# Optimization experiments

Measured on AMD Instinct MI355X. Metric: run time of the kernel, lower is better.

## Reference

```python
import jax, jax.numpy as jnp
import numpy as np

B, S, H, V, E = 64, 20, 128, 50257, 300


def gru(p, x, h):
    # tf.contrib.rnn.GRUCell: r,u = sigmoid([x,h]@Wg + bg); c = tanh([x, r*h]@Wc + bc); h' = u*h + (1-u)*c
    gk, gb, ck, cb = p
    xh = jnp.concatenate([x, h], axis=-1)
    r, u = jnp.split(jax.nn.sigmoid(xh @ gk + gb), 2, axis=-1)
    c = jnp.tanh(jnp.concatenate([x, r * h], axis=-1) @ ck + cb)
    return u * h + (1.0 - u) * c


def setup_inputs() -> dict:
    key = jax.random.key(0)
    ks = jax.random.split(key, 32)
    s = 0.08
    rn = lambda k, shp: (jax.random.normal(k, shp, jnp.float32) * s)
    inp = {}
    inp['x'] = jax.random.randint(ks[0], (B, S), 0, V, dtype=jnp.int32)
    inp['x_length'] = jax.random.randint(ks[1], (B,), 1, S + 1, dtype=jnp.int32)
    inp['y'] = jax.random.randint(ks[2], (B, S), 0, V, dtype=jnp.int32)
    inp['y_length'] = jax.random.randint(ks[3], (B,), 1, S + 1, dtype=jnp.int32)
    inp['embedding'] = jax.random.normal(ks[4], (V, E), jnp.float32) * 0.1
    # encoder GRU: layer0 in=E, layer1 in=H
    inp['e0_gk'] = rn(ks[5], (E + H, 2 * H)); inp['e0_gb'] = rn(ks[6], (2 * H,))
    inp['e0_ck'] = rn(ks[7], (E + H, H));     inp['e0_cb'] = rn(ks[8], (H,))
    inp['e1_gk'] = rn(ks[9], (2 * H, 2 * H)); inp['e1_gb'] = rn(ks[10], (2 * H,))
    inp['e1_ck'] = rn(ks[11], (2 * H, H));    inp['e1_cb'] = rn(ks[12], (H,))
    # decoder GRU: layer0 in = E + attention_size(H) = E+H, layer1 in=H
    inp['d0_gk'] = rn(ks[13], (E + 2 * H, 2 * H)); inp['d0_gb'] = rn(ks[14], (2 * H,))
    inp['d0_ck'] = rn(ks[15], (E + 2 * H, H));     inp['d0_cb'] = rn(ks[16], (H,))
    inp['d1_gk'] = rn(ks[17], (2 * H, 2 * H));     inp['d1_gb'] = rn(ks[18], (2 * H,))
    inp['d1_ck'] = rn(ks[19], (2 * H, H));         inp['d1_cb'] = rn(ks[20], (H,))
    # Bahdanau attention (num_units=H) + attention output layer + vocab projection
    inp['W_mem'] = rn(ks[21], (H, H))
    inp['W_q'] = rn(ks[22], (H, H))
    inp['v_att'] = rn(ks[23], (H,))
    inp['W_attn'] = rn(ks[24], (2 * H, H))
    inp['W_proj'] = rn(ks[25], (H, V))
    inp['b_proj'] = jnp.zeros((V,), jnp.float32)
    return inp


def _forward(x, x_length, y, y_length, embedding,
             e0_gk, e0_gb, e0_ck, e0_cb, e1_gk, e1_gb, e1_ck, e1_cb,
             d0_gk, d0_gb, d0_ck, d0_cb, d1_gk, d1_gb, d1_ck, d1_cb,
             W_mem, W_q, v_att, W_attn, W_proj, b_proj):
    e0 = (e0_gk, e0_gb, e0_ck, e0_cb)
    e1 = (e1_gk, e1_gb, e1_ck, e1_cb)
    d0 = (d0_gk, d0_gb, d0_ck, d0_cb)
    d1 = (d1_gk, d1_gb, d1_ck, d1_cb)
    t_idx = jnp.arange(S)
    x_valid = t_idx[None, :] < x_length[:, None]   # [B,S]
    y_valid = t_idx[None, :] < y_length[:, None]   # [B,S]

    # ---- encoder: 2-layer GRU dynamic_rnn with sequence_length semantics ----
    ex = embedding[x]                               # [B,S,E]
    zeros = jnp.zeros((x.shape[0], H), embedding.dtype)

    def enc_step(carry, inp_t):
        h0, h1 = carry
        xt, vt = inp_t                              # xt [B,E], vt [B,1]
        n0 = gru(e0, xt, h0)
        n1 = gru(e1, n0, h1)
        n0 = jnp.where(vt, n0, h0)                  # copy-through past seq end
        n1 = jnp.where(vt, n1, h1)
        return (n0, n1), jnp.where(vt, n1, 0.0)     # outputs zeroed past seq end

    (h0f, h1f), mem = jax.lax.scan(
        enc_step, (zeros, zeros),
        (ex.transpose(1, 0, 2), x_valid.T[:, :, None]))
    memory = mem.transpose(1, 0, 2)                 # [B,S,H] encoder outputs

    # ---- Bahdanau attention precompute ----
    keys = jnp.einsum('bsh,hu->bsu', memory, W_mem)  # memory_layer(memory)
    neg_inf = jnp.finfo(memory.dtype).min

    # ---- attention decoder (TrainingHelper) ----
    ey = embedding[y]                               # [B,S,E]
    attn0 = jnp.zeros((x.shape[0], H), embedding.dtype)

    def dec_step(carry, inp_t):
        h0, h1, attn = carry
        yt, vt = inp_t                              # yt [B,E], vt [B,1]
        ci = jnp.concatenate([yt, attn], axis=-1)   # cell input = [emb, prev attention]
        n0 = gru(d0, ci, h0)
        n1 = gru(d1, n0, h1)
        q = n1 @ W_q                                # query_layer(cell_output)
        sc = jnp.einsum('bsu,u->bs', jnp.tanh(keys + q[:, None, :]), v_att)
        sc = jnp.where(x_valid, sc, neg_inf)        # memory_sequence_length mask
        al = jax.nn.softmax(sc, axis=-1)            # [B,S]
        ctx = jnp.einsum('bs,bsh->bh', al, memory)  # context
        na = jnp.concatenate([n1, ctx], axis=-1) @ W_attn  # attention_layer (no bias)
        logits = na @ W_proj + b_proj               # projection_layer
        logits = jnp.where(vt, logits, 0.0)         # dynamic_decode zeroes finished emits
        return (n0, n1, na), logits

    _, logits = jax.lax.scan(
        dec_step, (h0f, h1f, attn0),
        (ey.transpose(1, 0, 2), y_valid.T[:, :, None]))
    return logits.transpose(1, 0, 2)                # [B,S,V] rnn_output


def reference(x, x_length, y, y_length, embedding,
              e0_gk, e0_gb, e0_ck, e0_cb, e1_gk, e1_gb, e1_ck, e1_cb,
              d0_gk, d0_gb, d0_ck, d0_cb, d1_gk, d1_gb, d1_ck, d1_cb,
              W_mem, W_q, v_att, W_attn, W_proj, b_proj):
    return _forward(x, x_length, y, y_length, embedding,
                    e0_gk, e0_gb, e0_ck, e0_cb, e1_gk, e1_gb, e1_ck, e1_cb,
                    d0_gk, d0_gb, d0_ck, d0_cb, d1_gk, d1_gb, d1_ck, d1_cb,
                    W_mem, W_q, v_att, W_attn, W_proj, b_proj)
```

## Files before the change

### kernel.cpp

```cpp
#include <hip/hip_runtime.h>
#include <hip/hip_bf16.h>

#define Bb 64
#define Ss 20
#define Hh 128
#define Vv 50257
#define Ee 300
#define Vpad 50304

typedef short bf16x8 __attribute__((ext_vector_type(8)));
typedef float f32x4 __attribute__((ext_vector_type(4)));

__device__ __forceinline__ unsigned short f2bf(float f){
  unsigned u = __float_as_uint(f);
  u += 0x7fff + ((u >> 16) & 1);
  return (unsigned short)(u >> 16);
}
__device__ __forceinline__ float sigm(float x){ return 1.f / (1.f + __expf(-x)); }
__device__ __forceinline__ float tanh_fast(float x){
  float e = __expf(2.f * x);
  return 1.f - 2.f / (e + 1.f);
}

template<int K4>
__device__ __forceinline__ float dotT(const float* __restrict__ w, const float* v){
  float a0 = 0.f, a1 = 0.f, a2 = 0.f, a3 = 0.f;
  const float4* w4 = (const float4*)w;
  const float4* v4 = (const float4*)v;
#pragma unroll
  for (int i = 0; i < K4; i++){
    float4 wv = w4[i]; float4 xv = v4[i];
    a0 = fmaf(wv.x, xv.x, a0); a1 = fmaf(wv.y, xv.y, a1);
    a2 = fmaf(wv.z, xv.z, a2); a3 = fmaf(wv.w, xv.w, a3);
  }
  return (a0 + a1) + (a2 + a3);
}


struct TMat { const float* src; float* dst; int r0, R, C; };
struct TList { TMat m[15]; };

__global__ __launch_bounds__(256) void wtrans_kernel(TList L){
  TMat t = L.m[blockIdx.y];
  int idx = blockIdx.x * 256 + threadIdx.x;
  int total = t.R * t.C;
  if (idx >= total) return;
  int o = idx / t.R;
  int i = idx - o * t.R;
  t.dst[idx] = t.src[(size_t)(t.r0 + i) * t.C + o];
}

__global__ __launch_bounds__(256) void wpt_kernel(const float* __restrict__ Wp,
                                                  unsigned short* __restrict__ Wpt){
  __shared__ unsigned short tile[64][136];
  int n0 = blockIdx.x * 64;
  int tid = threadIdx.x;
  for (int idx = tid; idx < 8192; idx += 256){
    int k = idx >> 6, nn = idx & 63;
    int n = n0 + nn;
    float f = (n < Vv) ? Wp[(size_t)k * Vv + n] : 0.f;
    tile[nn][k] = f2bf(f);
  }
  __syncthreads();
  for (int idx = tid; idx < 1024; idx += 256){
    int nn = idx >> 4, c = idx & 15;
    uint4 v = *reinterpret_cast<const uint4*>(&tile[nn][c * 8]);
    *reinterpret_cast<uint4*>(Wpt + (((size_t)(n0 + nn)) << 7) + c * 8) = v;
  }
}


__global__ __launch_bounds__(256) void pre_kernel(
    const int* __restrict__ x, const int* __restrict__ y, const float* __restrict__ emb,
    const float* __restrict__ egx, const float* __restrict__ ecx,
    const float* __restrict__ egb, const float* __restrict__ ecb,
    const float* __restrict__ dgx, const float* __restrict__ dcx,
    const float* __restrict__ dgb, const float* __restrict__ dcb,
    float* __restrict__ epg, float* __restrict__ epc,
    float* __restrict__ dpg, float* __restrict__ dpc)
{
  __shared__ __align__(16) float er[Ee];
  int tid = threadIdx.x, ti = blockIdx.x, which = blockIdx.y;
  int tok = which ? y[ti] : x[ti];
  if (tid < 75)
    ((float4*)er)[tid] = ((const float4*)(emb + (size_t)tok * Ee))[tid];
  __syncthreads();
  const float* gx = which ? dgx : egx;
  const float* cx = which ? dcx : ecx;
  float accg = (which ? dgb : egb)[tid] + dotT<75>(gx + (size_t)tid * Ee, er);
  (which ? dpg : epg)[ti * 256 + tid] = accg;
  if (tid < 128){
    float accc = (which ? dcb : ecb)[tid] + dotT<75>(cx + (size_t)tid * Ee, er);
    (which ? dpc : epc)[ti * 128 + tid] = accc;
  }
}


__global__ __launch_bounds__(256, 1) void recur2(
    const int* __restrict__ xlen,
    const float* __restrict__ epg, const float* __restrict__ epc,
    const float* __restrict__ dpg, const float* __restrict__ dpc,
    const float* __restrict__ e0_gh_t, const float* __restrict__ e0_ch_t,
    const float* __restrict__ e1_g_t, const float* __restrict__ e1_c_t,
    const float* __restrict__ e1_gb,  const float* __restrict__ e1_cb,
    const float* __restrict__ d0_gah_t, const float* __restrict__ d0_cah_t,
    const float* __restrict__ d1_g_t, const float* __restrict__ d1_c_t,
    const float* __restrict__ d1_gb,  const float* __restrict__ d1_cb,
    const float* __restrict__ W_mem_t, const float* __restrict__ W_q_t,
    const float* __restrict__ W_attn_t, const float* __restrict__ v_att,
    unsigned short* __restrict__ na_bf)
{
  __shared__ __align__(16) float mem_s[Ss][Hh];
  __shared__ __align__(16) float keys_s[Ss][132];
  __shared__ __align__(16) float h0[Hh], h1[Hh], attn[Hh], n0[Hh], n1[Hh], rh[Hh], q[Hh], ctx[Hh];
  __shared__ __align__(16) float gates[2*Hh];
  __shared__ __align__(16) float vatt_s[Hh];
  __shared__ float part[Ss][8], als[Ss];

  const int tid = threadIdx.x, b = blockIdx.x;
  if (tid < Hh){ h0[tid] = 0.f; h1[tid] = 0.f; attn[tid] = 0.f; vatt_s[tid] = v_att[tid]; }
  __syncthreads();
  const int xl = xlen[b];

  for (int t = 0; t < Ss; t++){
    const int tix = b * Ss + t;
    {
      float g = epg[(tix << 8) + tid] + dotT<32>(e0_gh_t + tid * 128, h0);
      float sg = sigm(g);
      if (tid < Hh) rh[tid] = sg * h0[tid];
      else          gates[tid] = sg;
    }
    __syncthreads();
    {
      int o = tid >> 1, half = tid & 1;
      float a = dotT<16>(e0_ch_t + o * 128 + half * 64, rh + half * 64);
      a += __shfl_xor(a, 1);
      if (!half){
        float c = tanh_fast(epc[(tix << 7) + o] + a);
        float u = gates[128 + o];
        n0[o] = u * h0[o] + (1.f - u) * c;
      }
    }
    __syncthreads();
    {
      float g1 = e1_gb[tid] + dotT<32>(e1_g_t + tid * 256, n0)
                            + dotT<32>(e1_g_t + tid * 256 + 128, h1);
      float sg = sigm(g1);
      if (tid < Hh) rh[tid] = sg * h1[tid];
      else          gates[tid] = sg;
    }
    __syncthreads();
    {
      int o = tid >> 1, half = tid & 1;
      const float* base = e1_c_t + o * 256 + half * 128;
      float a = half ? dotT<32>(base, rh) : dotT<32>(base, n0);
      a += __shfl_xor(a, 1);
      if (!half){
        float c = tanh_fast(e1_cb[o] + a);
        float u = gates[128 + o];
        float nh = u * h1[o] + (1.f - u) * c;
        bool v = (t < xl);
        mem_s[t][o] = v ? nh : 0.f;
        h1[o] = v ? nh : h1[o];
        h0[o] = v ? n0[o] : h0[o];
      }
    }
    __syncthreads();
  }

  for (int idx = tid; idx < Ss * Hh; idx += 256){
    int s = idx >> 7, j = idx & 127;
    keys_s[s][j] = dotT<32>(W_mem_t + j * 128, mem_s[s]);
  }
  __syncthreads();

  for (int t = 0; t < Ss; t++){
    const int tix = b * Ss + t;
    {
      float g = dpg[(tix << 8) + tid] + dotT<32>(d0_gah_t + tid * 256, attn)
                                      + dotT<32>(d0_gah_t + tid * 256 + 128, h0);
      float sg = sigm(g);
      if (tid < Hh) rh[tid] = sg * h0[tid];
      else          gates[tid] = sg;
    }
    __syncthreads();
    {
      int o = tid >> 1, half = tid & 1;
      const float* base = d0_cah_t + o * 256 + half * 128;
      float a = half ? dotT<32>(base, rh) : dotT<32>(base, attn);
      a += __shfl_xor(a, 1);
      if (!half){
        float c = tanh_fast(dpc[(tix << 7) + o] + a);
        float u = gates[128 + o];
        float nv = u * h0[o] + (1.f - u) * c;
        n0[o] = nv; h0[o] = nv;
      }
    }
    __syncthreads();
    {
      float g1 = d1_gb[tid] + dotT<32>(d1_g_t + tid * 256, n0)
                            + dotT<32>(d1_g_t + tid * 256 + 128, h1);
      float sg = sigm(g1);
      if (tid < Hh) rh[tid] = sg * h1[tid];
      else          gates[tid] = sg;
    }
    __syncthreads();
    {
      int o = tid >> 1, half = tid & 1;
      const float* base = d1_c_t + o * 256 + half * 128;
      float a = half ? dotT<32>(base, rh) : dotT<32>(base, n0);
      a += __shfl_xor(a, 1);
      if (!half){
        float c = tanh_fast(d1_cb[o] + a);
        float u = gates[128 + o];
        float nh = u * h1[o] + (1.f - u) * c;
        n1[o] = nh; h1[o] = nh;
      }
    }
    __syncthreads();
    {
      int o = tid >> 1, half = tid & 1;
      float a = dotT<16>(W_q_t + o * 128 + half * 64, n1 + half * 64);
      a += __shfl_xor(a, 1);
      if (!half) q[o] = a;
    }
    __syncthreads();
    if (tid < Ss * 8){
      int s = tid >> 3, p = tid & 7;
      float a = 0.f;
#pragma unroll
      for (int c2 = 0; c2 < 16; c2++){
        int u2 = p * 16 + c2;
        a += tanh_fast(keys_s[s][u2] + q[u2]) * vatt_s[u2];
      }
      part[s][p] = a;
    }
    __syncthreads();
    if (tid < 64){
      int s = tid;
      bool valid = (s < Ss) && (s < xl);
      float sc = -3.4e38f;
      if (valid){ sc = 0.f;
#pragma unroll
        for (int p = 0; p < 8; p++) sc += part[s][p];
      }
      float mx = sc;
#pragma unroll
      for (int off = 32; off >= 1; off >>= 1) mx = fmaxf(mx, __shfl_xor(mx, off));
      float e = valid ? __expf(sc - mx) : 0.f;
      float sm = e;
#pragma unroll
      for (int off = 32; off >= 1; off >>= 1) sm += __shfl_xor(sm, off);
      if (s < Ss) als[s] = e / sm;
    }
    __syncthreads();
    if (tid < Hh){
      float a = 0.f;
#pragma unroll
      for (int s = 0; s < Ss; s++) a += als[s] * mem_s[s][tid];
      ctx[tid] = a;
    }
    __syncthreads();
    {
      int o = tid >> 1, half = tid & 1;
      const float* base = W_attn_t + o * 256 + half * 128;
      float a = half ? dotT<32>(base, ctx) : dotT<32>(base, n1);
      a += __shfl_xor(a, 1);
      if (!half){
        attn[o] = a;
        na_bf[(tix << 7) + o] = f2bf(a);
      }
    }
    __syncthreads();
  }
}


__global__ __launch_bounds__(256) void proj2(
    const unsigned short* __restrict__ na_bf, const unsigned short* __restrict__ Wpt,
    const float* __restrict__ b_proj, const int* __restrict__ ylen,
    float* __restrict__ out)
{
  __shared__ int yl_s[Bb];
  const int tid = threadIdx.x;
  if (tid < Bb) yl_s[tid] = ylen[tid];
  const int n0 = blockIdx.x * 128, m0 = blockIdx.y * 64;
  const int lane = tid & 63, w = tid >> 6, lm = lane & 15, qq = lane >> 4;

  f32x4 acc[4][2];
#pragma unroll
  for (int mt = 0; mt < 4; mt++){ acc[mt][0] = (f32x4){0,0,0,0}; acc[mt][1] = (f32x4){0,0,0,0}; }

#pragma unroll
  for (int ks = 0; ks < 4; ks++){
    int ko = ks * 32 + qq * 8;
    bf16x8 b0 = *(const bf16x8*)(Wpt + (((size_t)(n0 + w*32 + lm)) << 7) + ko);
    bf16x8 b1 = *(const bf16x8*)(Wpt + (((size_t)(n0 + w*32 + 16 + lm)) << 7) + ko);
#pragma unroll
    for (int mt = 0; mt < 4; mt++){
      bf16x8 a = *(const bf16x8*)(na_bf + (((size_t)(m0 + mt*16 + lm)) << 7) + ko);
      acc[mt][0] = __builtin_amdgcn_mfma_f32_16x16x32_bf16(a, b0, acc[mt][0], 0, 0, 0);
      acc[mt][1] = __builtin_amdgcn_mfma_f32_16x16x32_bf16(a, b1, acc[mt][1], 0, 0, 0);
    }
  }
  __syncthreads();

#pragma unroll
  for (int mt = 0; mt < 4; mt++){
    int row = m0 + mt*16 + qq*4;
#pragma unroll
    for (int n2 = 0; n2 < 2; n2++){
      int col = n0 + w*32 + n2*16 + lm;
      if (col < Vv){
        float bp = b_proj[col];
#pragma unroll
        for (int r = 0; r < 4; r++){
          int rr = row + r;
          int bb = rr / Ss;
          int tt = rr - bb * Ss;
          float val = (tt < yl_s[bb]) ? (acc[mt][n2][r] + bp) : 0.f;
          out[(size_t)rr * Vv + col] = val;
        }
      }
    }
  }
}

extern "C" void kernel_launch(void* const* d_in, const int* in_sizes, int n_in,
                              void* d_out, int out_size, void* d_ws, size_t ws_size,
                              hipStream_t stream) {
  const int*   x        = (const int*)d_in[0];
  const int*   x_length = (const int*)d_in[1];
  const int*   y        = (const int*)d_in[2];
  const int*   y_length = (const int*)d_in[3];
  const float* emb      = (const float*)d_in[4];
  const float* e0_gk = (const float*)d_in[5];  const float* e0_gb = (const float*)d_in[6];
  const float* e0_ck = (const float*)d_in[7];  const float* e0_cb = (const float*)d_in[8];
  const float* e1_gk = (const float*)d_in[9];  const float* e1_gb = (const float*)d_in[10];
  const float* e1_ck = (const float*)d_in[11]; const float* e1_cb = (const float*)d_in[12];
  const float* d0_gk = (const float*)d_in[13]; const float* d0_gb = (const float*)d_in[14];
  const float* d0_ck = (const float*)d_in[15]; const float* d0_cb = (const float*)d_in[16];
  const float* d1_gk = (const float*)d_in[17]; const float* d1_gb = (const float*)d_in[18];
  const float* d1_ck = (const float*)d_in[19]; const float* d1_cb = (const float*)d_in[20];
  const float* W_mem = (const float*)d_in[21]; const float* W_q   = (const float*)d_in[22];
  const float* v_att = (const float*)d_in[23]; const float* W_attn= (const float*)d_in[24];
  const float* W_proj= (const float*)d_in[25]; const float* b_proj= (const float*)d_in[26];
  float* out = (float*)d_out;

  size_t off = 0;
  auto alloc = [&](size_t bytes) -> void* {
    void* p = (char*)d_ws + off;
    off += (bytes + 255) & ~(size_t)255;
    return p;
  };
  unsigned short* Wpt   = (unsigned short*)alloc((size_t)Vpad * 128 * 2);
  unsigned short* na_bf = (unsigned short*)alloc((size_t)Bb * Ss * Hh * 2);
  float* epg = (float*)alloc((size_t)Bb*Ss*256*4);
  float* epc = (float*)alloc((size_t)Bb*Ss*128*4);
  float* dpg = (float*)alloc((size_t)Bb*Ss*256*4);
  float* dpc = (float*)alloc((size_t)Bb*Ss*128*4);
  float* e0_gx_t  = (float*)alloc(256*300*4);
  float* e0_gh_t  = (float*)alloc(256*128*4);
  float* e0_cx_t  = (float*)alloc(128*300*4);
  float* e0_ch_t  = (float*)alloc(128*128*4);
  float* e1_g_t   = (float*)alloc(256*256*4);
  float* e1_c_t   = (float*)alloc(128*256*4);
  float* d0_gx_t  = (float*)alloc(256*300*4);
  float* d0_gah_t = (float*)alloc(256*256*4);
  float* d0_cx_t  = (float*)alloc(128*300*4);
  float* d0_cah_t = (float*)alloc(128*256*4);
  float* d1_g_t   = (float*)alloc(256*256*4);
  float* d1_c_t   = (float*)alloc(128*256*4);
  float* W_mem_t  = (float*)alloc(128*128*4);
  float* W_q_t    = (float*)alloc(128*128*4);
  float* W_attn_t = (float*)alloc(128*256*4);

  TList L;
  L.m[0]  = { e0_gk, e0_gx_t,    0, 300, 256 };
  L.m[1]  = { e0_gk, e0_gh_t,  300, 128, 256 };
  L.m[2]  = { e0_ck, e0_cx_t,    0, 300, 128 };
  L.m[3]  = { e0_ck, e0_ch_t,  300, 128, 128 };
  L.m[4]  = { e1_gk, e1_g_t,     0, 256, 256 };
  L.m[5]  = { e1_ck, e1_c_t,     0, 256, 128 };
  L.m[6]  = { d0_gk, d0_gx_t,    0, 300, 256 };
  L.m[7]  = { d0_gk, d0_gah_t, 300, 256, 256 };
  L.m[8]  = { d0_ck, d0_cx_t,    0, 300, 128 };
  L.m[9]  = { d0_ck, d0_cah_t, 300, 256, 128 };
  L.m[10] = { d1_gk, d1_g_t,     0, 256, 256 };
  L.m[11] = { d1_ck, d1_c_t,     0, 256, 128 };
  L.m[12] = { W_mem, W_mem_t,    0, 128, 128 };
  L.m[13] = { W_q,   W_q_t,      0, 128, 128 };
  L.m[14] = { W_attn,W_attn_t,   0, 256, 128 };

  wtrans_kernel<<<dim3(300, 15), 256, 0, stream>>>(L);
  wpt_kernel<<<Vpad / 64, 256, 0, stream>>>(W_proj, Wpt);
  pre_kernel<<<dim3(Bb * Ss, 2), 256, 0, stream>>>(
      x, y, emb, e0_gx_t, e0_cx_t, e0_gb, e0_cb,
      d0_gx_t, d0_cx_t, d0_gb, d0_cb, epg, epc, dpg, dpc);
  recur2<<<Bb, 256, 0, stream>>>(
      x_length, epg, epc, dpg, dpc,
      e0_gh_t, e0_ch_t, e1_g_t, e1_c_t, e1_gb, e1_cb,
      d0_gah_t, d0_cah_t, d1_g_t, d1_c_t, d1_gb, d1_cb,
      W_mem_t, W_q_t, W_attn_t, v_att, na_bf);
  proj2<<<dim3(Vpad / 128, (Bb * Ss) / 64), 256, 0, stream>>>(
      na_bf, Wpt, b_proj, y_length, out);
}
```

Baseline: 1.331 ms.

## Double recurrence block to 512 threads and fuse softmax into context step

The sequential GRU/attention recurrence kernel now runs with 512 threads per block. Each matvec is split across two or four threads per output with shuffle reductions, which shortens the per-thread dot-product chain on the serial critical path. The separate softmax stage with its barrier is removed, and each context thread now recomputes max, exp and sum redundantly. This saves a sync per decoder step at the cost of duplicated work and more wavefronts per block.

```diff
diff --git a/kernel.cpp b/kernel.cpp
--- a/kernel.cpp
+++ b/kernel.cpp
@@ -96,7 +96,7 @@
 }
 
 
-__global__ __launch_bounds__(256, 1) void recur2(
+__global__ __launch_bounds__(512, 1) void recur2(
     const int* __restrict__ xlen,
     const float* __restrict__ epg, const float* __restrict__ epc,
     const float* __restrict__ dpg, const float* __restrict__ dpc,
@@ -115,60 +115,67 @@
   __shared__ __align__(16) float h0[Hh], h1[Hh], attn[Hh], n0[Hh], n1[Hh], rh[Hh], q[Hh], ctx[Hh];
   __shared__ __align__(16) float gates[2*Hh];
   __shared__ __align__(16) float vatt_s[Hh];
-  __shared__ float part[Ss][8], als[Ss];
+  __shared__ float part[Ss][8];
 
   const int tid = threadIdx.x, b = blockIdx.x;
   if (tid < Hh){ h0[tid] = 0.f; h1[tid] = 0.f; attn[tid] = 0.f; vatt_s[tid] = v_att[tid]; }
   __syncthreads();
   const int xl = xlen[b];
 
+  const int o2 = tid >> 1, hf = tid & 1;
+  const int o4 = tid >> 2, qu = tid & 3;
+
   for (int t = 0; t < Ss; t++){
     const int tix = b * Ss + t;
     {
-      float g = epg[(tix << 8) + tid] + dotT<32>(e0_gh_t + tid * 128, h0);
-      float sg = sigm(g);
-      if (tid < Hh) rh[tid] = sg * h0[tid];
-      else          gates[tid] = sg;
-    }
-    __syncthreads();
-    {
-      int o = tid >> 1, half = tid & 1;
-      float a = dotT<16>(e0_ch_t + o * 128 + half * 64, rh + half * 64);
+      float a = dotT<16>(e0_gh_t + o2 * 128 + hf * 64, h0 + hf * 64);
       a += __shfl_xor(a, 1);
-      if (!half){
-        float c = tanh_fast(epc[(tix << 7) + o] + a);
-        float u = gates[128 + o];
-        n0[o] = u * h0[o] + (1.f - u) * c;
-      }
-    }
-    __syncthreads();
-    {
-      float g1 = e1_gb[tid] + dotT<32>(e1_g_t + tid * 256, n0)
-                            + dotT<32>(e1_g_t + tid * 256 + 128, h1);
-      float sg = sigm(g1);
-      if (tid < Hh) rh[tid] = sg * h1[tid];
-      else          gates[tid] = sg;
-    }
-    __syncthreads();
-    {
-      int o = tid >> 1, half = tid & 1;
-      const float* base = e1_c_t + o * 256 + half * 128;
-      float a = half ? dotT<32>(base, rh) : dotT<32>(base, n0);
+      if (!hf){
+        float sg = sigm(epg[(tix << 8) + o2] + a);
+        if (o2 < Hh) rh[o2] = sg * h0[o2];
+        else         gates[o2] = sg;
+      }
+    }
+    __syncthreads();
+    {
+      float a = dotT<8>(e0_ch_t + o4 * 128 + qu * 32, rh + qu * 32);
+      a += __shfl_xor(a, 1); a += __shfl_xor(a, 2);
+      if (!qu){
+        float c = tanh_fast(epc[(tix << 7) + o4] + a);
+        float u = gates[128 + o4];
+        n0[o4] = u * h0[o4] + (1.f - u) * c;
+      }
+    }
+    __syncthreads();
+    {
+      const float* base = e1_g_t + o2 * 256 + hf * 128;
+      float a = hf ? dotT<32>(base, h1) : dotT<32>(base, n0);
       a += __shfl_xor(a, 1);
-      if (!half){
-        float c = tanh_fast(e1_cb[o] + a);
-        float u = gates[128 + o];
-        float nh = u * h1[o] + (1.f - u) * c;
-        bool v = (t < xl);
-        mem_s[t][o] = v ? nh : 0.f;
-        h1[o] = v ? nh : h1[o];
-        h0[o] = v ? n0[o] : h0[o];
-      }
-    }
-    __syncthreads();
-  }
-
-  for (int idx = tid; idx < Ss * Hh; idx += 256){
+      if (!hf){
+        float sg = sigm(e1_gb[o2] + a);
+        if (o2 < Hh) rh[o2] = sg * h1[o2];
+        else         gates[o2] = sg;
+      }
+    }
+    __syncthreads();
+    {
+      const float* v = (qu < 2) ? n0 : rh;
+      float a = dotT<16>(e1_c_t + o4 * 256 + qu * 64, v + (qu & 1) * 64);
+      a += __shfl_xor(a, 1); a += __shfl_xor(a, 2);
+      if (!qu){
+        float c = tanh_fast(e1_cb[o4] + a);
+        float u = gates[128 + o4];
+        float nh = u * h1[o4] + (1.f - u) * c;
+        bool vv = (t < xl);
+        mem_s[t][o4] = vv ? nh : 0.f;
+        h1[o4] = vv ? nh : h1[o4];
+        h0[o4] = vv ? n0[o4] : h0[o4];
+      }
+    }
+    __syncthreads();
+  }
+
+  for (int idx = tid; idx < Ss * Hh; idx += 512){
     int s = idx >> 7, j = idx & 127;
     keys_s[s][j] = dotT<32>(W_mem_t + j * 128, mem_s[s]);
   }
@@ -177,52 +184,55 @@
   for (int t = 0; t < Ss; t++){
     const int tix = b * Ss + t;
     {
-      float g = dpg[(tix << 8) + tid] + dotT<32>(d0_gah_t + tid * 256, attn)
-                                      + dotT<32>(d0_gah_t + tid * 256 + 128, h0);
-      float sg = sigm(g);
-      if (tid < Hh) rh[tid] = sg * h0[tid];
-      else          gates[tid] = sg;
-    }
-    __syncthreads();
-    {
-      int o = tid >> 1, half = tid & 1;
-      const float* base = d0_cah_t + o * 256 + half * 128;
-      float a = half ? dotT<32>(base, rh) : dotT<32>(base, attn);
+      const float* base = d0_gah_t + o2 * 256 + hf * 128;
+      float a = hf ? dotT<32>(base, h0) : dotT<32>(base, attn);
       a += __shfl_xor(a, 1);
-      if (!half){
-        float c = tanh_fast(dpc[(tix << 7) + o] + a);
-        float u = gates[128 + o];
-        float nv = u * h0[o] + (1.f - u) * c;
-        n0[o] = nv; h0[o] = nv;
-      }
-    }
-    __syncthreads();
-    {
-      float g1 = d1_gb[tid] + dotT<32>(d1_g_t + tid * 256, n0)
-                            + dotT<32>(d1_g_t + tid * 256 + 128, h1);
-      float sg = sigm(g1);
-      if (tid < Hh) rh[tid] = sg * h1[tid];
-      else          gates[tid] = sg;
-    }
-    __syncthreads();
-    {
-      int o = tid >> 1, half = tid & 1;
-      const float* base = d1_c_t + o * 256 + half * 128;
-      float a = half ? dotT<32>(base, rh) : dotT<32>(base, n0);
+      if (!hf){
+        float sg = sigm(dpg[(tix << 8) + o2] + a);
+        if (o2 < Hh) rh[o2] = sg * h0[o2];
+        else         gates[o2] = sg;
+      }
+    }
+    __syncthreads();
+    {
+      const float* v = (qu < 2) ? attn : rh;
+      float a = dotT<16>(d0_cah_t + o4 * 256 + qu * 64, v + (qu & 1) * 64);
+      a += __shfl_xor(a, 1); a += __shfl_xor(a, 2);
+      if (!qu){
+        float c = tanh_fast(dpc[(tix << 7) + o4] + a);
+        float u = gates[128 + o4];
+        float nv = u * h0[o4] + (1.f - u) * c;
+        n0[o4] = nv; h0[o4] = nv;
+      }
+    }
+    __syncthreads();
+    {
+      const float* base = d1_g_t + o2 * 256 + hf * 128;
+      float a = hf ? dotT<32>(base, h1) : dotT<32>(base, n0);
       a += __shfl_xor(a, 1);
-      if (!half){
-        float c = tanh_fast(d1_cb[o] + a);
-        float u = gates[128 + o];
-        float nh = u * h1[o] + (1.f - u) * c;
-        n1[o] = nh; h1[o] = nh;
-      }
-    }
-    __syncthreads();
-    {
-      int o = tid >> 1, half = tid & 1;
-      float a = dotT<16>(W_q_t + o * 128 + half * 64, n1 + half * 64);
-      a += __shfl_xor(a, 1);
-      if (!half) q[o] = a;
+      if (!hf){
+        float sg = sigm(d1_gb[o2] + a);
+        if (o2 < Hh) rh[o2] = sg * h1[o2];
+        else         gates[o2] = sg;
+      }
+    }
+    __syncthreads();
+    {
+      const float* v = (qu < 2) ? n0 : rh;
+      float a = dotT<16>(d1_c_t + o4 * 256 + qu * 64, v + (qu & 1) * 64);
+      a += __shfl_xor(a, 1); a += __shfl_xor(a, 2);
+      if (!qu){
+        float c = tanh_fast(d1_cb[o4] + a);
+        float u = gates[128 + o4];
+        float nh = u * h1[o4] + (1.f - u) * c;
+        n1[o4] = nh; h1[o4] = nh;
+      }
+    }
+    __syncthreads();
+    {
+      float a = dotT<8>(W_q_t + o4 * 128 + qu * 32, n1 + qu * 32);
+      a += __shfl_xor(a, 1); a += __shfl_xor(a, 2);
+      if (!qu) q[o4] = a;
     }
     __syncthreads();
     if (tid < Ss * 8){
@@ -236,39 +246,36 @@
       part[s][p] = a;
     }
     __syncthreads();
-    if (tid < 64){
-      int s = tid;
-      bool valid = (s < Ss) && (s < xl);
-      float sc = -3.4e38f;
-      if (valid){ sc = 0.f;
-#pragma unroll
-        for (int p = 0; p < 8; p++) sc += part[s][p];
-      }
-      float mx = sc;
-#pragma unroll
-      for (int off = 32; off >= 1; off >>= 1) mx = fmaxf(mx, __shfl_xor(mx, off));
-      float e = valid ? __expf(sc - mx) : 0.f;
-      float sm = e;
-#pragma unroll
-      for (int off = 32; off >= 1; off >>= 1) sm += __shfl_xor(sm, off);
-      if (s < Ss) als[s] = e / sm;
-    }
-    __syncthreads();
     if (tid < Hh){
+      float e_[Ss];
+      float mx = -3.4e38f;
+#pragma unroll
+      for (int s = 0; s < Ss; s++){
+        float v = ((part[s][0] + part[s][1]) + (part[s][2] + part[s][3]))
+                + ((part[s][4] + part[s][5]) + (part[s][6] + part[s][7]));
+        v = (s < xl) ? v : -3.4e38f;
+        e_[s] = v; mx = fmaxf(mx, v);
+      }
+      float sm = 0.f;
+#pragma unroll
+      for (int s = 0; s < Ss; s++){
+        float e = (s < xl) ? __expf(e_[s] - mx) : 0.f;
+        e_[s] = e; sm += e;
+      }
+      float inv = 1.f / sm;
       float a = 0.f;
 #pragma unroll
-      for (int s = 0; s < Ss; s++) a += als[s] * mem_s[s][tid];
-      ctx[tid] = a;
-    }
-    __syncthreads();
-    {
-      int o = tid >> 1, half = tid & 1;
-      const float* base = W_attn_t + o * 256 + half * 128;
-      float a = half ? dotT<32>(base, ctx) : dotT<32>(base, n1);
-      a += __shfl_xor(a, 1);
-      if (!half){
-        attn[o] = a;
-        na_bf[(tix << 7) + o] = f2bf(a);
+      for (int s = 0; s < Ss; s++) a = fmaf(e_[s], mem_s[s][tid], a);
+      ctx[tid] = a * inv;
+    }
+    __syncthreads();
+    {
+      const float* v = (qu < 2) ? n1 : ctx;
+      float a = dotT<16>(W_attn_t + o4 * 256 + qu * 64, v + (qu & 1) * 64);
+      a += __shfl_xor(a, 1); a += __shfl_xor(a, 2);
+      if (!qu){
+        attn[o4] = a;
+        na_bf[(tix << 7) + o4] = f2bf(a);
       }
     }
     __syncthreads();
@@ -397,7 +404,7 @@
   pre_kernel<<<dim3(Bb * Ss, 2), 256, 0, stream>>>(
       x, y, emb, e0_gx_t, e0_cx_t, e0_gb, e0_cb,
       d0_gx_t, d0_cx_t, d0_gb, d0_cb, epg, epc, dpg, dpc);
-  recur2<<<Bb, 256, 0, stream>>>(
+  recur2<<<Bb, 512, 0, stream>>>(
       x_length, epg, epc, dpg, dpc,
       e0_gh_t, e0_ch_t, e1_g_t, e1_c_t, e1_gb, e1_cb,
       d0_gah_t, d0_cah_t, d1_g_t, d1_c_t, d1_gb, d1_cb,
```

After: 1.434 ms. 7.8% more time.

## Store recurrent weights in fp16 and fuse attention softmax into context step

Applied to the files above, without the earlier changes.

Recurrent and attention weight matrices are transposed into fp16 instead of fp32, and the sequential recurrence kernel reads them with 8-wide half loads converted to float. This halves the weight bytes streamed each timestep, which is meant to ease the latency- and bandwidth-bound serial loop. The attention softmax is also folded into the context computation, with each thread recomputing it redundantly, which removes one barrier per decoder step. The cost is reduced weight precision, which could shift numerics against the fp32 reference.

```diff
diff --git a/kernel.cpp b/kernel.cpp
--- a/kernel.cpp
+++ b/kernel.cpp
@@ -1,5 +1,6 @@
 #include <hip/hip_runtime.h>
 #include <hip/hip_bf16.h>
+#include <hip/hip_fp16.h>
 
 #define Bb 64
 #define Ss 20
@@ -10,6 +11,7 @@
 
 typedef short bf16x8 __attribute__((ext_vector_type(8)));
 typedef float f32x4 __attribute__((ext_vector_type(4)));
+typedef _Float16 h16x8 __attribute__((ext_vector_type(8)));
 
 __device__ __forceinline__ unsigned short f2bf(float f){
   unsigned u = __float_as_uint(f);
@@ -36,8 +38,25 @@
   return (a0 + a1) + (a2 + a3);
 }
 
-
-struct TMat { const float* src; float* dst; int r0, R, C; };
+template<int K8>
+__device__ __forceinline__ float dotH(const _Float16* __restrict__ w, const float* v){
+  float a0 = 0.f, a1 = 0.f, a2 = 0.f, a3 = 0.f;
+  const h16x8* w8 = (const h16x8*)w;
+  const float4* v4 = (const float4*)v;
+#pragma unroll
+  for (int i = 0; i < K8; i++){
+    h16x8 hv = w8[i];
+    float4 x0 = v4[2*i], x1 = v4[2*i+1];
+    a0 = fmaf((float)hv[0], x0.x, a0); a1 = fmaf((float)hv[1], x0.y, a1);
+    a2 = fmaf((float)hv[2], x0.z, a2); a3 = fmaf((float)hv[3], x0.w, a3);
+    a0 = fmaf((float)hv[4], x1.x, a0); a1 = fmaf((float)hv[5], x1.y, a1);
+    a2 = fmaf((float)hv[6], x1.z, a2); a3 = fmaf((float)hv[7], x1.w, a3);
+  }
+  return (a0 + a1) + (a2 + a3);
+}
+
+
+struct TMat { const float* src; void* dst; int r0, R, C, h; };
 struct TList { TMat m[15]; };
 
 __global__ __launch_bounds__(256) void wtrans_kernel(TList L){
@@ -47,7 +66,9 @@
   if (idx >= total) return;
   int o = idx / t.R;
   int i = idx - o * t.R;
-  t.dst[idx] = t.src[(size_t)(t.r0 + i) * t.C + o];
+  float val = t.src[(size_t)(t.r0 + i) * t.C + o];
+  if (t.h) ((_Float16*)t.dst)[idx] = (_Float16)val;
+  else     ((float*)t.dst)[idx]    = val;
 }
 
 __global__ __launch_bounds__(256) void wpt_kernel(const float* __restrict__ Wp,
@@ -100,14 +121,14 @@
     const int* __restrict__ xlen,
     const float* __restrict__ epg, const float* __restrict__ epc,
     const float* __restrict__ dpg, const float* __restrict__ dpc,
-    const float* __restrict__ e0_gh_t, const float* __restrict__ e0_ch_t,
-    const float* __restrict__ e1_g_t, const float* __restrict__ e1_c_t,
+    const _Float16* __restrict__ e0_gh_h, const _Float16* __restrict__ e0_ch_h,
+    const _Float16* __restrict__ e1_g_h, const _Float16* __restrict__ e1_c_h,
     const float* __restrict__ e1_gb,  const float* __restrict__ e1_cb,
-    const float* __restrict__ d0_gah_t, const float* __restrict__ d0_cah_t,
-    const float* __restrict__ d1_g_t, const float* __restrict__ d1_c_t,
+    const _Float16* __restrict__ d0_gah_h, const _Float16* __restrict__ d0_cah_h,
+    const _Float16* __restrict__ d1_g_h, const _Float16* __restrict__ d1_c_h,
     const float* __restrict__ d1_gb,  const float* __restrict__ d1_cb,
-    const float* __restrict__ W_mem_t, const float* __restrict__ W_q_t,
-    const float* __restrict__ W_attn_t, const float* __restrict__ v_att,
+    const _Float16* __restrict__ W_mem_h, const _Float16* __restrict__ W_q_h,
+    const _Float16* __restrict__ W_attn_h, const float* __restrict__ v_att,
     unsigned short* __restrict__ na_bf)
 {
   __shared__ __align__(16) float mem_s[Ss][Hh];
@@ -115,25 +136,25 @@
   __shared__ __align__(16) float h0[Hh], h1[Hh], attn[Hh], n0[Hh], n1[Hh], rh[Hh], q[Hh], ctx[Hh];
   __shared__ __align__(16) float gates[2*Hh];
   __shared__ __align__(16) float vatt_s[Hh];
-  __shared__ float part[Ss][8], als[Ss];
+  __shared__ float part[Ss][8];
 
   const int tid = threadIdx.x, b = blockIdx.x;
   if (tid < Hh){ h0[tid] = 0.f; h1[tid] = 0.f; attn[tid] = 0.f; vatt_s[tid] = v_att[tid]; }
   __syncthreads();
   const int xl = xlen[b];
+  const int o = tid >> 1, half = tid & 1;
 
   for (int t = 0; t < Ss; t++){
     const int tix = b * Ss + t;
     {
-      float g = epg[(tix << 8) + tid] + dotT<32>(e0_gh_t + tid * 128, h0);
+      float g = epg[(tix << 8) + tid] + dotH<16>(e0_gh_h + tid * 128, h0);
       float sg = sigm(g);
       if (tid < Hh) rh[tid] = sg * h0[tid];
       else          gates[tid] = sg;
     }
     __syncthreads();
     {
-      int o = tid >> 1, half = tid & 1;
-      float a = dotT<16>(e0_ch_t + o * 128 + half * 64, rh + half * 64);
+      float a = dotH<8>(e0_ch_h + o * 128 + half * 64, rh + half * 64);
       a += __shfl_xor(a, 1);
       if (!half){
         float c = tanh_fast(epc[(tix << 7) + o] + a);
@@ -143,17 +164,16 @@
     }
     __syncthreads();
     {
-      float g1 = e1_gb[tid] + dotT<32>(e1_g_t + tid * 256, n0)
-                            + dotT<32>(e1_g_t + tid * 256 + 128, h1);
+      float g1 = e1_gb[tid] + dotH<16>(e1_g_h + tid * 256, n0)
+                            + dotH<16>(e1_g_h + tid * 256 + 128, h1);
       float sg = sigm(g1);
       if (tid < Hh) rh[tid] = sg * h1[tid];
       else          gates[tid] = sg;
     }
     __syncthreads();
     {
-      int o = tid >> 1, half = tid & 1;
-      const float* base = e1_c_t + o * 256 + half * 128;
-      float a = half ? dotT<32>(base, rh) : dotT<32>(base, n0);
+      const _Float16* base = e1_c_h + o * 256 + half * 128;
+      float a = half ? dotH<16>(base, rh) : dotH<16>(base, n0);
       a += __shfl_xor(a, 1);
       if (!half){
         float c = tanh_fast(e1_cb[o] + a);
@@ -170,24 +190,23 @@
 
   for (int idx = tid; idx < Ss * Hh; idx += 256){
     int s = idx >> 7, j = idx & 127;
-    keys_s[s][j] = dotT<32>(W_mem_t + j * 128, mem_s[s]);
+    keys_s[s][j] = dotH<16>(W_mem_h + j * 128, mem_s[s]);
   }
   __syncthreads();
 
   for (int t = 0; t < Ss; t++){
     const int tix = b * Ss + t;
     {
-      float g = dpg[(tix << 8) + tid] + dotT<32>(d0_gah_t + tid * 256, attn)
-                                      + dotT<32>(d0_gah_t + tid * 256 + 128, h0);
+      float g = dpg[(tix << 8) + tid] + dotH<16>(d0_gah_h + tid * 256, attn)
+                                      + dotH<16>(d0_gah_h + tid * 256 + 128, h0);
       float sg = sigm(g);
       if (tid < Hh) rh[tid] = sg * h0[tid];
       else          gates[tid] = sg;
     }
     __syncthreads();
     {
-      int o = tid >> 1, half = tid & 1;
-      const float* base = d0_cah_t + o * 256 + half * 128;
-      float a = half ? dotT<32>(base, rh) : dotT<32>(base, attn);
+      const _Float16* base = d0_cah_h + o * 256 + half * 128;
+      float a = half ? dotH<16>(base, rh) : dotH<16>(base, attn);
       a += __shfl_xor(a, 1);
       if (!half){
         float c = tanh_fast(dpc[(tix << 7) + o] + a);
@@ -198,17 +217,16 @@
     }
     __syncthreads();
     {
-      float g1 = d1_gb[tid] + dotT<32>(d1_g_t + tid * 256, n0)
-                            + dotT<32>(d1_g_t + tid * 256 + 128, h1);
+      float g1 = d1_gb[tid] + dotH<16>(d1_g_h + tid * 256, n0)
+                            + dotH<16>(d1_g_h + tid * 256 + 128, h1);
       float sg = sigm(g1);
       if (tid < Hh) rh[tid] = sg * h1[tid];
       else          gates[tid] = sg;
     }
     __syncthreads();
     {
-      int o = tid >> 1, half = tid & 1;
-      const float* base = d1_c_t + o * 256 + half * 128;
-      float a = half ? dotT<32>(base, rh) : dotT<32>(base, n0);
+      const _Float16* base = d1_c_h + o * 256 + half * 128;
+      float a = half ? dotH<16>(base, rh) : dotH<16>(base, n0);
       a += __shfl_xor(a, 1);
       if (!half){
         float c = tanh_fast(d1_cb[o] + a);
@@ -219,8 +237,7 @@
     }
     __syncthreads();
     {
-      int o = tid >> 1, half = tid & 1;
-      float a = dotT<16>(W_q_t + o * 128 + half * 64, n1 + half * 64);
+      float a = dotH<8>(W_q_h + o * 128 + half * 64, n1 + half * 64);
       a += __shfl_xor(a, 1);
       if (!half) q[o] = a;
     }
@@ -236,35 +253,32 @@
       part[s][p] = a;
     }
     __syncthreads();
-    if (tid < 64){
-      int s = tid;
-      bool valid = (s < Ss) && (s < xl);
-      float sc = -3.4e38f;
-      if (valid){ sc = 0.f;
-#pragma unroll
-        for (int p = 0; p < 8; p++) sc += part[s][p];
-      }
-      float mx = sc;
-#pragma unroll
-      for (int off = 32; off >= 1; off >>= 1) mx = fmaxf(mx, __shfl_xor(mx, off));
-      float e = valid ? __expf(sc - mx) : 0.f;
-      float sm = e;
-#pragma unroll
-      for (int off = 32; off >= 1; off >>= 1) sm += __shfl_xor(sm, off);
-      if (s < Ss) als[s] = e / sm;
-    }
-    __syncthreads();
     if (tid < Hh){
+      float e_[Ss];
+      float mx = -3.4e38f;
+#pragma unroll
+      for (int s = 0; s < Ss; s++){
+        float v = ((part[s][0] + part[s][1]) + (part[s][2] + part[s][3]))
+                + ((part[s][4] + part[s][5]) + (part[s][6] + part[s][7]));
+        v = (s < xl) ? v : -3.4e38f;
+        e_[s] = v; mx = fmaxf(mx, v);
+      }
+      float sm = 0.f;
+#pragma unroll
+      for (int s = 0; s < Ss; s++){
+        float e = (s < xl) ? __expf(e_[s] - mx) : 0.f;
+        e_[s] = e; sm += e;
+      }
+      float inv = 1.f / sm;
       float a = 0.f;
 #pragma unroll
-      for (int s = 0; s < Ss; s++) a += als[s] * mem_s[s][tid];
-      ctx[tid] = a;
-    }
-    __syncthreads();
-    {
-      int o = tid >> 1, half = tid & 1;
-      const float* base = W_attn_t + o * 256 + half * 128;
-      float a = half ? dotT<32>(base, ctx) : dotT<32>(base, n1);
+      for (int s = 0; s < Ss; s++) a = fmaf(e_[s], mem_s[s][tid], a);
+      ctx[tid] = a * inv;
+    }
+    __syncthreads();
+    {
+      const _Float16* base = W_attn_h + o * 256 + half * 128;
+      float a = half ? dotH<16>(base, ctx) : dotH<16>(base, n1);
       a += __shfl_xor(a, 1);
       if (!half){
         attn[o] = a;
@@ -360,37 +374,37 @@
   float* dpg = (float*)alloc((size_t)Bb*Ss*256*4);
   float* dpc = (float*)alloc((size_t)Bb*Ss*128*4);
   float* e0_gx_t  = (float*)alloc(256*300*4);
-  float* e0_gh_t  = (float*)alloc(256*128*4);
   float* e0_cx_t  = (float*)alloc(128*300*4);
-  float* e0_ch_t  = (float*)alloc(128*128*4);
-  float* e1_g_t   = (float*)alloc(256*256*4);
-  float* e1_c_t   = (float*)alloc(128*256*4);
   float* d0_gx_t  = (float*)alloc(256*300*4);
-  float* d0_gah_t = (float*)alloc(256*256*4);
   float* d0_cx_t  = (float*)alloc(128*300*4);
-  float* d0_cah_t = (float*)alloc(128*256*4);
-  float* d1_g_t   = (float*)alloc(256*256*4);
-  float* d1_c_t   = (float*)alloc(128*256*4);
-  float* W_mem_t  = (float*)alloc(128*128*4);
-  float* W_q_t    = (float*)alloc(128*128*4);
-  float* W_attn_t = (float*)alloc(128*256*4);
+  _Float16* e0_gh_h  = (_Float16*)alloc(256*128*2);
+  _Float16* e0_ch_h  = (_Float16*)alloc(128*128*2);
+  _Float16* e1_g_h   = (_Float16*)alloc(256*256*2);
+  _Float16* e1_c_h   = (_Float16*)alloc(128*256*2);
+  _Float16* d0_gah_h = (_Float16*)alloc(256*256*2);
+  _Float16* d0_cah_h = (_Float16*)alloc(128*256*2);
+  _Float16* d1_g_h   = (_Float16*)alloc(256*256*2);
+  _Float16* d1_c_h   = (_Float16*)alloc(128*256*2);
+  _Float16* W_mem_h  = (_Float16*)alloc(128*128*2);
+  _Float16* W_q_h    = (_Float16*)alloc(128*128*2);
+  _Float16* W_attn_h = (_Float16*)alloc(128*256*2);
 
   TList L;
-  L.m[0]  = { e0_gk, e0_gx_t,    0, 300, 256 };
-  L.m[1]  = { e0_gk, e0_gh_t,  300, 128, 256 };
-  L.m[2]  = { e0_ck, e0_cx_t,    0, 300, 128 };
-  L.m[3]  = { e0_ck, e0_ch_t,  300, 128, 128 };
-  L.m[4]  = { e1_gk, e1_g_t,     0, 256, 256 };
-  L.m[5]  = { e1_ck, e1_c_t,     0, 256, 128 };
-  L.m[6]  = { d0_gk, d0_gx_t,    0, 300, 256 };
-  L.m[7]  = { d0_gk, d0_gah_t, 300, 256, 256 };
-  L.m[8]  = { d0_ck, d0_cx_t,    0, 300, 128 };
-  L.m[9]  = { d0_ck, d0_cah_t, 300, 256, 128 };
-  L.m[10] = { d1_gk, d1_g_t,     0, 256, 256 };
-  L.m[11] = { d1_ck, d1_c_t,     0, 256, 128 };
-  L.m[12] = { W_mem, W_mem_t,    0, 128, 128 };
-  L.m[13] = { W_q,   W_q_t,      0, 128, 128 };
-  L.m[14] = { W_attn,W_attn_t,   0, 256, 128 };
+  L.m[0]  = { e0_gk, e0_gx_t,    0, 300, 256, 0 };
+  L.m[1]  = { e0_gk, e0_gh_h,  300, 128, 256, 1 };
+  L.m[2]  = { e0_ck, e0_cx_t,    0, 300, 128, 0 };
+  L.m[3]  = { e0_ck, e0_ch_h,  300, 128, 128, 1 };
+  L.m[4]  = { e1_gk, e1_g_h,     0, 256, 256, 1 };
+  L.m[5]  = { e1_ck, e1_c_h,     0, 256, 128, 1 };
+  L.m[6]  = { d0_gk, d0_gx_t,    0, 300, 256, 0 };
+  L.m[7]  = { d0_gk, d0_gah_h, 300, 256, 256, 1 };
+  L.m[8]  = { d0_ck, d0_cx_t,    0, 300, 128, 0 };
+  L.m[9]  = { d0_ck, d0_cah_h, 300, 256, 128, 1 };
+  L.m[10] = { d1_gk, d1_g_h,     0, 256, 256, 1 };
+  L.m[11] = { d1_ck, d1_c_h,     0, 256, 128, 1 };
+  L.m[12] = { W_mem, W_mem_h,    0, 128, 128, 1 };
+  L.m[13] = { W_q,   W_q_h,      0, 128, 128, 1 };
+  L.m[14] = { W_attn,W_attn_h,   0, 256, 128, 1 };
 
   wtrans_kernel<<<dim3(300, 15), 256, 0, stream>>>(L);
   wpt_kernel<<<Vpad / 64, 256, 0, stream>>>(W_proj, Wpt);
@@ -399,9 +413,9 @@
       d0_gx_t, d0_cx_t, d0_gb, d0_cb, epg, epc, dpg, dpc);
   recur2<<<Bb, 256, 0, stream>>>(
       x_length, epg, epc, dpg, dpc,
-      e0_gh_t, e0_ch_t, e1_g_t, e1_c_t, e1_gb, e1_cb,
-      d0_gah_t, d0_cah_t, d1_g_t, d1_c_t, d1_gb, d1_cb,
-      W_mem_t, W_q_t, W_attn_t, v_att, na_bf);
+      e0_gh_h, e0_ch_h, e1_g_h, e1_c_h, e1_gb, e1_cb,
+      d0_gah_h, d0_cah_h, d1_g_h, d1_c_h, d1_gb, d1_cb,
+      W_mem_h, W_q_h, W_attn_h, v_att, na_bf);
   proj2<<<dim3(Vpad / 128, (Bb * Ss) / 64), 256, 0, stream>>>(
       na_bf, Wpt, b_proj, y_length, out);
 }
```

After: 1.461 ms. +9.8%, slower.

## Use lane-coalesced weight reads with wave shuffle reductions in recurrent GEMVs

Applied to the files above, without the earlier changes.

Replaces per-thread row dot products, where each thread strides through its own weight row, with a wave-cooperative GEMV: lanes read consecutive float4s of a row (coalesced), reduce with xor shuffles, and the owning lane keeps the result. The softmax step is also merged into the context computation, so every thread recomputes the max and sum itself and one barrier is dropped. This trades uncoalesced global loads for many more shuffle instructions per output, which could cost more than it saves if the weights were already cache-resident.

```diff
diff --git a/kernel.cpp b/kernel.cpp
--- a/kernel.cpp
+++ b/kernel.cpp
@@ -21,6 +21,9 @@
   float e = __expf(2.f * x);
   return 1.f - 2.f / (e + 1.f);
 }
+__device__ __forceinline__ float dot4(float4 a, float4 b){
+  return fmaf(a.x, b.x, fmaf(a.y, b.y, fmaf(a.z, b.z, a.w * b.w)));
+}
 
 template<int K4>
 __device__ __forceinline__ float dotT(const float* __restrict__ w, const float* v){
@@ -34,6 +37,55 @@
     a2 = fmaf(wv.z, xv.z, a2); a3 = fmaf(wv.w, xv.w, a3);
   }
   return (a0 + a1) + (a2 + a3);
+}
+
+__device__ __forceinline__ float gemvG256(const float* __restrict__ W, int wv, int l, float4 vr){
+  const float4* w4 = (const float4*)W;
+  float acc = 0.f;
+#pragma unroll
+  for (int j = 0; j < 64; j++){
+    float p = dot4(w4[(wv*64 + j)*64 + l], vr);
+    p += __shfl_xor(p,32); p += __shfl_xor(p,16); p += __shfl_xor(p,8);
+    p += __shfl_xor(p,4);  p += __shfl_xor(p,2);  p += __shfl_xor(p,1);
+    if (l == j) acc = p;
+  }
+  return acc;
+}
+__device__ __forceinline__ float gemvG128(const float* __restrict__ W, int wv, int l, float4 vr){
+  const float4* w4 = (const float4*)W;
+  float acc = 0.f;
+#pragma unroll
+  for (int j = 0; j < 32; j++){
+    float p = dot4(w4[(wv*64 + 2*j)*32 + l], vr);
+    p += __shfl_xor(p,16); p += __shfl_xor(p,8); p += __shfl_xor(p,4);
+    p += __shfl_xor(p,2);  p += __shfl_xor(p,1);
+    if ((l & 31) == j) acc = p;
+  }
+  return acc;
+}
+__device__ __forceinline__ float gemvC256(const float* __restrict__ W, int wv, int l, float4 vr){
+  const float4* w4 = (const float4*)W;
+  float acc = 0.f;
+#pragma unroll
+  for (int j = 0; j < 32; j++){
+    float p = dot4(w4[(wv*32 + j)*64 + l], vr);
+    p += __shfl_xor(p,32); p += __shfl_xor(p,16); p += __shfl_xor(p,8);
+    p += __shfl_xor(p,4);  p += __shfl_xor(p,2);  p += __shfl_xor(p,1);
+    if (l == j) acc = p;
+  }
+  return acc;
+}
+__device__ __forceinline__ float gemvC128(const float* __restrict__ W, int wv, int l, float4 vr){
+  const float4* w4 = (const float4*)W;
+  float acc = 0.f;
+#pragma unroll
+  for (int j = 0; j < 16; j++){
+    float p = dot4(w4[(wv*32 + 2*j)*32 + l], vr);
+    p += __shfl_xor(p,16); p += __shfl_xor(p,8); p += __shfl_xor(p,4);
+    p += __shfl_xor(p,2);  p += __shfl_xor(p,1);
+    if ((l & 31) == j) acc = p;
+  }
+  return acc;
 }
 
 
@@ -115,27 +167,41 @@
   __shared__ __align__(16) float h0[Hh], h1[Hh], attn[Hh], n0[Hh], n1[Hh], rh[Hh], q[Hh], ctx[Hh];
   __shared__ __align__(16) float gates[2*Hh];
   __shared__ __align__(16) float vatt_s[Hh];
-  __shared__ float part[Ss][8], als[Ss];
+  __shared__ float part[Ss][8];
 
   const int tid = threadIdx.x, b = blockIdx.x;
   if (tid < Hh){ h0[tid] = 0.f; h1[tid] = 0.f; attn[tid] = 0.f; vatt_s[tid] = v_att[tid]; }
   __syncthreads();
   const int xl = xlen[b];
+  const int l = tid & 63, wv = tid >> 6;
+  const int oG128 = wv*64 + 2*(l & 31) + (l >> 5);
+  const int oG256 = tid;
+  const int oC    = wv*32 + l;
+  const int oC128 = wv*32 + 2*(l & 31) + (l >> 5);
+
+  const float4* h0_4   = (const float4*)h0;
+  const float4* h1_4   = (const float4*)h1;
+  const float4* n0_4   = (const float4*)n0;
+  const float4* n1_4   = (const float4*)n1;
+  const float4* rh_4   = (const float4*)rh;
+  const float4* at_4   = (const float4*)attn;
+  const float4* ctx_4  = (const float4*)ctx;
 
   for (int t = 0; t < Ss; t++){
     const int tix = b * Ss + t;
     {
-      float g = epg[(tix << 8) + tid] + dotT<32>(e0_gh_t + tid * 128, h0);
+      float4 vr = h0_4[l & 31];
+      float g = epg[(tix << 8) + oG128] + gemvG128(e0_gh_t, wv, l, vr);
       float sg = sigm(g);
-      if (tid < Hh) rh[tid] = sg * h0[tid];
-      else          gates[tid] = sg;
-    }
-    __syncthreads();
-    {
-      int o = tid >> 1, half = tid & 1;
-      float a = dotT<16>(e0_ch_t + o * 128 + half * 64, rh + half * 64);
-      a += __shfl_xor(a, 1);
-      if (!half){
+      if (oG128 < Hh) rh[oG128] = sg * h0[oG128];
+      else            gates[oG128] = sg;
+    }
+    __syncthreads();
+    {
+      float4 vr = rh_4[l & 31];
+      float a = gemvC128(e0_ch_t, wv, l, vr);
+      if ((l & 31) < 16){
+        int o = oC128;
         float c = tanh_fast(epc[(tix << 7) + o] + a);
         float u = gates[128 + o];
         n0[o] = u * h0[o] + (1.f - u) * c;
@@ -143,19 +209,18 @@
     }
     __syncthreads();
     {
-      float g1 = e1_gb[tid] + dotT<32>(e1_g_t + tid * 256, n0)
-                            + dotT<32>(e1_g_t + tid * 256 + 128, h1);
+      float4 vr = (l < 32) ? n0_4[l] : h1_4[l & 31];
+      float g1 = e1_gb[oG256] + gemvG256(e1_g_t, wv, l, vr);
       float sg = sigm(g1);
-      if (tid < Hh) rh[tid] = sg * h1[tid];
-      else          gates[tid] = sg;
-    }
-    __syncthreads();
-    {
-      int o = tid >> 1, half = tid & 1;
-      const float* base = e1_c_t + o * 256 + half * 128;
-      float a = half ? dotT<32>(base, rh) : dotT<32>(base, n0);
-      a += __shfl_xor(a, 1);
-      if (!half){
+      if (oG256 < Hh) rh[oG256] = sg * h1[oG256];
+      else            gates[oG256] = sg;
+    }
+    __syncthreads();
+    {
+      float4 vr = (l < 32) ? n0_4[l] : rh_4[l & 31];
+      float a = gemvC256(e1_c_t, wv, l, vr);
+      if (l < 32){
+        int o = oC;
         float c = tanh_fast(e1_cb[o] + a);
         float u = gates[128 + o];
         float nh = u * h1[o] + (1.f - u) * c;
@@ -177,19 +242,18 @@
   for (int t = 0; t < Ss; t++){
     const int tix = b * Ss + t;
     {
-      float g = dpg[(tix << 8) + tid] + dotT<32>(d0_gah_t + tid * 256, attn)
-                                      + dotT<32>(d0_gah_t + tid * 256 + 128, h0);
+      float4 vr = (l < 32) ? at_4[l] : h0_4[l & 31];
+      float g = dpg[(tix << 8) + oG256] + gemvG256(d0_gah_t, wv, l, vr);
       float sg = sigm(g);
-      if (tid < Hh) rh[tid] = sg * h0[tid];
-      else          gates[tid] = sg;
-    }
-    __syncthreads();
-    {
-      int o = tid >> 1, half = tid & 1;
-      const float* base = d0_cah_t + o * 256 + half * 128;
-      float a = half ? dotT<32>(base, rh) : dotT<32>(base, attn);
-      a += __shfl_xor(a, 1);
-      if (!half){
+      if (oG256 < Hh) rh[oG256] = sg * h0[oG256];
+      else            gates[oG256] = sg;
+    }
+    __syncthreads();
+    {
+      float4 vr = (l < 32) ? at_4[l] : rh_4[l & 31];
+      float a = gemvC256(d0_cah_t, wv, l, vr);
+      if (l < 32){
+        int o = oC;
         float c = tanh_fast(dpc[(tix << 7) + o] + a);
         float u = gates[128 + o];
         float nv = u * h0[o] + (1.f - u) * c;
@@ -198,19 +262,18 @@
     }
     __syncthreads();
     {
-      float g1 = d1_gb[tid] + dotT<32>(d1_g_t + tid * 256, n0)
-                            + dotT<32>(d1_g_t + tid * 256 + 128, h1);
+      float4 vr = (l < 32) ? n0_4[l] : h1_4[l & 31];
+      float g1 = d1_gb[oG256] + gemvG256(d1_g_t, wv, l, vr);
       float sg = sigm(g1);
-      if (tid < Hh) rh[tid] = sg * h1[tid];
-      else          gates[tid] = sg;
-    }
-    __syncthreads();
-    {
-      int o = tid >> 1, half = tid & 1;
-      const float* base = d1_c_t + o * 256 + half * 128;
-      float a = half ? dotT<32>(base, rh) : dotT<32>(base, n0);
-      a += __shfl_xor(a, 1);
-      if (!half){
+      if (oG256 < Hh) rh[oG256] = sg * h1[oG256];
+      else            gates[oG256] = sg;
+    }
+    __syncthreads();
+    {
+      float4 vr = (l < 32) ? n0_4[l] : rh_4[l & 31];
+      float a = gemvC256(d1_c_t, wv, l, vr);
+      if (l < 32){
+        int o = oC;
         float c = tanh_fast(d1_cb[o] + a);
         float u = gates[128 + o];
         float nh = u * h1[o] + (1.f - u) * c;
@@ -219,10 +282,9 @@
     }
     __syncthreads();
     {
-      int o = tid >> 1, half = tid & 1;
-      float a = dotT<16>(W_q_t + o * 128 + half * 64, n1 + half * 64);
-      a += __shfl_xor(a, 1);
-      if (!half) q[o] = a;
+      float4 vr = n1_4[l & 31];
+      float a = gemvC128(W_q_t, wv, l, vr);
+      if ((l & 31) < 16) q[oC128] = a;
     }
     __syncthreads();
     if (tid < Ss * 8){
@@ -236,37 +298,34 @@
       part[s][p] = a;
     }
     __syncthreads();
-    if (tid < 64){
-      int s = tid;
-      bool valid = (s < Ss) && (s < xl);
-      float sc = -3.4e38f;
-      if (valid){ sc = 0.f;
-#pragma unroll
-        for (int p = 0; p < 8; p++) sc += part[s][p];
-      }
-      float mx = sc;
-#pragma unroll
-      for (int off = 32; off >= 1; off >>= 1) mx = fmaxf(mx, __shfl_xor(mx, off));
-      float e = valid ? __expf(sc - mx) : 0.f;
-      float sm = e;
-#pragma unroll
-      for (int off = 32; off >= 1; off >>= 1) sm += __shfl_xor(sm, off);
-      if (s < Ss) als[s] = e / sm;
-    }
-    __syncthreads();
     if (tid < Hh){
+      float e_[Ss];
+      float mx = -3.4e38f;
+#pragma unroll
+      for (int s = 0; s < Ss; s++){
+        float v = ((part[s][0] + part[s][1]) + (part[s][2] + part[s][3]))
+                + ((part[s][4] + part[s][5]) + (part[s][6] + part[s][7]));
+        v = (s < xl) ? v : -3.4e38f;
+        e_[s] = v; mx = fmaxf(mx, v);
+      }
+      float sm = 0.f;
+#pragma unroll
+      for (int s = 0; s < Ss; s++){
+        float e = (s < xl) ? __expf(e_[s] - mx) : 0.f;
+        e_[s] = e; sm += e;
+      }
+      float inv = 1.f / sm;
       float a = 0.f;
 #pragma unroll
-      for (int s = 0; s < Ss; s++) a += als[s] * mem_s[s][tid];
-      ctx[tid] = a;
-    }
-    __syncthreads();
-    {
-      int o = tid >> 1, half = tid & 1;
-      const float* base = W_attn_t + o * 256 + half * 128;
-      float a = half ? dotT<32>(base, ctx) : dotT<32>(base, n1);
-      a += __shfl_xor(a, 1);
-      if (!half){
+      for (int s = 0; s < Ss; s++) a = fmaf(e_[s], mem_s[s][tid], a);
+      ctx[tid] = a * inv;
+    }
+    __syncthreads();
+    {
+      float4 vr = (l < 32) ? n1_4[l] : ctx_4[l & 31];
+      float a = gemvC256(W_attn_t, wv, l, vr);
+      if (l < 32){
+        int o = oC;
         attn[o] = a;
         na_bf[(tix << 7) + o] = f2bf(a);
       }
```

Result: slower. 2.531 ms (+90.2%).
